# Performance work log

Measured on AMD Instinct MI355X. Metric: run time of the kernel, lower is better.

The kernel has to match this reference:

```python
import jax, jax.numpy as jnp
import numpy as np

NUM_EXPERTS = 8
HIDDEN = 2048
FFN = 1376
CAPACITY_FACTOR = 1.25
SCORE_SCALE = 1.0


def setup_inputs() -> dict:
    key = jax.random.key(0)
    k = jax.random.split(key, 6)
    T = 8192
    x = jax.random.normal(k[0], (T, HIDDEN), dtype=jnp.float32)
    topK_indices = jax.random.randint(k[1], (T,), 0, NUM_EXPERTS, dtype=jnp.int64)
    topK_scores = jax.random.uniform(k[2], (T,), dtype=jnp.float32)
    s = 1.0 / np.sqrt(HIDDEN)
    w_gate = jax.random.normal(k[3], (NUM_EXPERTS, HIDDEN, FFN), dtype=jnp.float32) * s
    w_up = jax.random.normal(k[4], (NUM_EXPERTS, HIDDEN, FFN), dtype=jnp.float32) * s
    w_down = jax.random.normal(k[5], (NUM_EXPERTS, FFN, HIDDEN), dtype=jnp.float32) * (1.0 / np.sqrt(FFN))
    return {"x": x, "topK_indices": topK_indices, "topK_scores": topK_scores,
            "w_gate": w_gate, "w_up": w_up, "w_down": w_down}


def reference(x, topK_indices, topK_scores, w_gate, w_up, w_down):
    T, D = x.shape
    E = w_gate.shape[0]
    capacity = int(CAPACITY_FACTOR * T / E)  # static (depends only on shapes)
    # position of each token within its assigned expert (deterministic drop:
    # keep the first `capacity` tokens in sequence order per expert)
    oh = jax.nn.one_hot(topK_indices, E, dtype=jnp.int32)          # [T,E]
    rank = jnp.take_along_axis(jnp.cumsum(oh, axis=0) - 1,
                               topK_indices[:, None].astype(jnp.int32), axis=1)[:, 0]
    keep = rank < capacity                                          # [T]
    # dispatch into per-expert capacity buffers; dropped tokens go to dummy slot
    slot = jnp.where(keep, topK_indices.astype(jnp.int32) * capacity + rank, E * capacity)
    buf = jnp.zeros((E * capacity + 1, D), x.dtype)
    buf = buf.at[slot].set(jnp.where(keep[:, None], x, jnp.zeros_like(x)))
    xe = buf[:E * capacity].reshape(E, capacity, D)                 # [E,C,D]
    # per-expert SwiGLU MLP as grouped GEMMs
    h = jax.nn.silu(jnp.einsum('ecd,edf->ecf', xe, w_gate)) * jnp.einsum('ecd,edf->ecf', xe, w_up)
    out = jnp.einsum('ecf,efd->ecd', h, w_down).reshape(E * capacity, D)
    out = jnp.concatenate([out, jnp.zeros((1, D), out.dtype)], axis=0)
    # combine: dropped tokens -> zero (dropped_padding='zero'), gate-score fusion
    y = out[slot] * keep[:, None].astype(out.dtype)
    y = y * (topK_scores[:, None] * SCORE_SCALE)
    return y
```

## Files before the change

### kernel.cpp

```cpp
#include <hip/hip_runtime.h>
#include <hip/hip_bf16.h>
#include <cstdint>
#include <cstddef>

#define NTOK 8192
#define DH   2048
#define DF   1376
#define DFP  1408
#define NE   8
#define CAP  1280

typedef __bf16 bf16x8 __attribute__((ext_vector_type(8)));
typedef float  f32x4  __attribute__((ext_vector_type(4)));

#define BARRIER() asm volatile("s_barrier" ::: "memory")
#define WAITV(n)  asm volatile("s_waitcnt vmcnt(" #n ")" ::: "memory")
#define SETPRIO(n) __builtin_amdgcn_s_setprio(n)

__device__ __forceinline__ uint32_t pk2(float a, float b) {
  float2 f; f.x = a; f.y = b;
  union { __hip_bfloat162 h; uint32_t u; } cv;
  cv.h = __float22bfloat162_rn(f);
  return cv.u;
}
__device__ __forceinline__ ushort bf16bits(float a) {
  return (ushort)(pk2(a, 0.f) & 0xFFFFu);
}
__device__ __forceinline__ void gload16(const ushort* g, ushort* l) {
  __builtin_amdgcn_global_load_lds(
      (const __attribute__((address_space(1))) uint32_t*)(const void*)g,
      (__attribute__((address_space(3))) uint32_t*)(void*)l,
      16, 0, 0);
}

__device__ __forceinline__ void rp_src(int o, int& row, int& ko) {
  int p = o >> 7;
  int g = ((o >> 4) & 7) ^ (p & 7);
  row = p * 2 + (g >> 2);
  ko  = (g & 3) * 8;
}
__device__ __forceinline__ int rp_off(int row, int l4) {
  return ((row >> 1) << 7) + (((((row & 1) << 2) + l4) ^ ((row >> 1) & 7)) << 4);
}

__global__ void routing_kernel(const int* __restrict__ idx, int* __restrict__ tok_slot,
                               int* __restrict__ tok_keep) {
  __shared__ int cnt[256][NE];
  const int t = threadIdx.x;
  for (int s = t; s < NE * CAP; s += 256) tok_slot[s] = -1;
  unsigned long long cA = 0ull, cB = 0ull;
  const int per = NTOK / 256, base = t * per;
  for (int i = 0; i < per; ++i) {
    int e = idx[base + i];
    unsigned long long inc = 1ull << ((e & 3) * 16);
    if (e < 4) cA += inc; else cB += inc;
  }
#pragma unroll
  for (int e = 0; e < 4; ++e) cnt[t][e]     = (int)((cA >> (e * 16)) & 0xFFFF);
#pragma unroll
  for (int e = 0; e < 4; ++e) cnt[t][4 + e] = (int)((cB >> (e * 16)) & 0xFFFF);
  __syncthreads();
  if (t < NE) {
    int run = 0;
    for (int i = 0; i < 256; ++i) { int c = cnt[i][t]; cnt[i][t] = run; run += c; }
  }
  __syncthreads();
  cA = 0ull; cB = 0ull;
#pragma unroll
  for (int e = 0; e < 4; ++e) cA |= (unsigned long long)(cnt[t][e] & 0xFFFF) << (e * 16);
#pragma unroll
  for (int e = 0; e < 4; ++e) cB |= (unsigned long long)(cnt[t][4 + e] & 0xFFFF) << (e * 16);
  for (int i = 0; i < per; ++i) {
    int token = base + i;
    int e = idx[token];
    int sh = (e & 3) * 16;
    int r = (int)(((e < 4 ? cA : cB) >> sh) & 0xFFFF);
    unsigned long long inc = 1ull << sh;
    if (e < 4) cA += inc; else cB += inc;
    bool keep = (r < CAP);
    tok_keep[token] = keep ? 1 : 0;
    if (keep) tok_slot[e * CAP + r] = token;
  }
}

__global__ void zero_dropped(const int* __restrict__ keep, float* __restrict__ y) {
  if (keep[blockIdx.x]) return;
  float4 z = {0.f, 0.f, 0.f, 0.f};
  float* p = y + (size_t)blockIdx.x * DH + threadIdx.x * 8;
  *(float4*)p = z;
  *(float4*)(p + 4) = z;
}

__global__ void convert_x(const float* __restrict__ x, ushort* __restrict__ xb) {
  int i = (blockIdx.x * 256 + threadIdx.x) * 8;
  float4 a = *(const float4*)(x + i);
  float4 b = *(const float4*)(x + i + 4);
  uint4 p = { pk2(a.x, a.y), pk2(a.z, a.w), pk2(b.x, b.y), pk2(b.z, b.w) };
  *(uint4*)(xb + i) = p;
}

__global__ __launch_bounds__(256) void transpose_cvt(
    const float* __restrict__ in, ushort* __restrict__ out, int K, int N) {
  __shared__ ushort T[64][72];
  const int tid = threadIdx.x;
  const int n0 = blockIdx.x * 64, k0 = blockIdx.y * 64;
  const size_t eoff_in  = (size_t)blockIdx.z * K * N;
  const size_t eoff_out = (size_t)blockIdx.z * N * K;
  const int kr = tid >> 4;
  const int nc = (tid & 15) * 4;
#pragma unroll
  for (int it = 0; it < 4; ++it) {
    int k = k0 + kr + it * 16;
    int n = n0 + nc;
    float4 v = {0.f, 0.f, 0.f, 0.f};
    if (k < K && n + 4 <= N) v = *(const float4*)(in + eoff_in + (size_t)k * N + n);
    T[nc + 0][kr + it * 16] = bf16bits(v.x);
    T[nc + 1][kr + it * 16] = bf16bits(v.y);
    T[nc + 2][kr + it * 16] = bf16bits(v.z);
    T[nc + 3][kr + it * 16] = bf16bits(v.w);
  }
  __syncthreads();
  const int nr = tid >> 2;
  const int kc = tid & 3;
#pragma unroll
  for (int it = 0; it < 2; ++it) {
    int kloc = kc * 16 + it * 8;
    int n = n0 + nr, k = k0 + kloc;
    if (n < N && k + 8 <= K)
      *(uint4*)(out + eoff_out + (size_t)n * K + k) = *(const uint4*)&T[nr][kloc];
  }
}

__global__ void pad_h(ushort* __restrict__ h) {
  int idx = blockIdx.x * 512 + threadIdx.x;
  int row = idx >> 2, q = idx & 3;
  uint4 z = {0u, 0u, 0u, 0u};
  *(uint4*)(h + (size_t)row * DFP + DF + q * 8) = z;
}

__global__ __launch_bounds__(512, 1) void gemm_gateup3(
    const ushort* __restrict__ xb, const ushort* __restrict__ wgt,
    const ushort* __restrict__ wut, const int* __restrict__ tok_slot,
    ushort* __restrict__ h)
{
  __shared__ __align__(16) char sm[131072];
  const int tid = threadIdx.x, lane = tid & 63, wid = tid >> 6;
  const int wr = wid >> 1, wc = wid & 1;
  const int l15 = lane & 15, l4 = lane >> 4;

  int wgid = (blockIdx.x & 7) * 55 + (blockIdx.x >> 3);
  const int e = wgid / 55;
  const int rem = wgid - e * 55;
  const int mt = rem / 11, nt = rem - (rem / 11) * 11;
  const int n0 = nt * 128;

  const ushort* srcA[2]; const ushort* srcBg; const ushort* srcBu;
#pragma unroll
  for (int c = 0; c < 2; ++c) {
    int o = c * 8192 + wid * 1024 + lane * 16;
    int row, ko; rp_src(o, row, ko);
    int tk = tok_slot[e * CAP + mt * 256 + row];
    if (tk < 0) tk = 0;
    srcA[c] = xb + (size_t)tk * DH + ko;
  }
  {
    int o = wid * 1024 + lane * 16;
    int row, ko; rp_src(o, row, ko);
    int n = n0 + row; if (n > DF - 1) n = DF - 1;
    srcBg = wgt + ((size_t)e * DF + n) * DH + ko;
    srcBu = wut + ((size_t)e * DF + n) * DH + ko;
  }
  int aoff[4], boff[4];
#pragma unroll
  for (int i = 0; i < 4; ++i) aoff[i] = rp_off(wr * 64 + i * 16 + l15, l4);
#pragma unroll
  for (int j = 0; j < 4; ++j) boff[j] = rp_off(wc * 64 + j * 16 + l15, l4);
  const int dstw = wid * 1024;

  f32x4 accG[4][4], accU[4][4];
#pragma unroll
  for (int i = 0; i < 4; ++i)
#pragma unroll
    for (int j = 0; j < 4; ++j) {
      accG[i][j] = (f32x4){0.f, 0.f, 0.f, 0.f};
      accU[i][j] = (f32x4){0.f, 0.f, 0.f, 0.f};
    }

  const int NT = DH / 32;
#pragma unroll
  for (int t0 = 0; t0 < 3; ++t0) {
    int kk = t0 * 32;
    gload16(srcA[0] + kk, (ushort*)(sm + t0 * 16384 + dstw));
    gload16(srcA[1] + kk, (ushort*)(sm + t0 * 16384 + 8192 + dstw));
    gload16(srcBg   + kk, (ushort*)(sm + 65536 + t0 * 8192 + dstw));
    gload16(srcBu   + kk, (ushort*)(sm + 98304 + t0 * 8192 + dstw));
  }
  WAITV(8);
  BARRIER();

  for (int t = 0; t < NT; ++t) {
    const int r = t & 3, w = (t + 3) & 3;
    char* Ab  = sm + r * 16384;
    char* Bgb = sm + 65536 + r * 8192;
    char* Bub = sm + 98304 + r * 8192;
    bf16x8 a[4], bg[4], bu[4];
#pragma unroll
    for (int i = 0; i < 4; ++i) a[i]  = *(const bf16x8*)(Ab + aoff[i]);
#pragma unroll
    for (int j = 0; j < 4; ++j) bg[j] = *(const bf16x8*)(Bgb + boff[j]);
#pragma unroll
    for (int j = 0; j < 4; ++j) bu[j] = *(const bf16x8*)(Bub + boff[j]);
    if (t + 3 < NT) {
      int kk = (t + 3) * 32;
      gload16(srcA[0] + kk, (ushort*)(sm + w * 16384 + dstw));
      gload16(srcA[1] + kk, (ushort*)(sm + w * 16384 + 8192 + dstw));
      gload16(srcBg   + kk, (ushort*)(sm + 65536 + w * 8192 + dstw));
      gload16(srcBu   + kk, (ushort*)(sm + 98304 + w * 8192 + dstw));
    }
    SETPRIO(1);
#pragma unroll
    for (int j = 0; j < 4; ++j)
#pragma unroll
      for (int i = 0; i < 4; ++i)
        accG[i][j] = __builtin_amdgcn_mfma_f32_16x16x32_bf16(a[i], bg[j], accG[i][j], 0, 0, 0);
#pragma unroll
    for (int j = 0; j < 4; ++j)
#pragma unroll
      for (int i = 0; i < 4; ++i)
        accU[i][j] = __builtin_amdgcn_mfma_f32_16x16x32_bf16(a[i], bu[j], accU[i][j], 0, 0, 0);
    SETPRIO(0);
    if (t + 3 < NT)      { WAITV(8); }
    else if (t + 2 < NT) { WAITV(4); }
    else if (t + 1 < NT) { WAITV(0); }
    BARRIER();
  }
  const size_t rowbase = (size_t)(e * CAP + mt * 256 + wr * 64);
#pragma unroll
  for (int j = 0; j < 4; ++j) {
    int col = n0 + wc * 64 + j * 16 + l15;
    if (col < DF) {
#pragma unroll
      for (int i = 0; i < 4; ++i)
#pragma unroll
        for (int r2 = 0; r2 < 4; ++r2) {
          size_t row = rowbase + i * 16 + l4 * 4 + r2;
          float gv = accG[i][j][r2], uv = accU[i][j][r2];
          h[row * DFP + col] = bf16bits(gv / (1.f + __expf(-gv)) * uv);
        }
    }
  }
}

__global__ __launch_bounds__(512, 1) void gemm_down3(
    const ushort* __restrict__ h, const ushort* __restrict__ wdt,
    const int* __restrict__ tok_slot, const float* __restrict__ scores,
    float* __restrict__ y)
{
  __shared__ __align__(16) char sm[100352];
  int* tokc = (int*)(sm + 98304);
  float* scc = (float*)(sm + 99328);
  const int tid = threadIdx.x, lane = tid & 63, wid = tid >> 6;
  const int wr = wid >> 1, wc = wid & 1;
  const int l15 = lane & 15, l4 = lane >> 4;

  int wgid = (blockIdx.x & 7) * 80 + (blockIdx.x >> 3);
  const int e = wgid / 80;
  const int rem = wgid - e * 80;
  const int mt = rem / 16, nt = rem & 15;
  const int n0 = nt * 128;

  if (tid < 256) {
    int tk = tok_slot[e * CAP + mt * 256 + tid];
    tokc[tid] = tk;
    scc[tid] = (tk >= 0) ? scores[tk] : 0.f;
  }
  __syncthreads();

  const size_t hrow0 = (size_t)(e * CAP + mt * 256);
  const ushort* srcA[2]; const ushort* srcB;
#pragma unroll
  for (int c = 0; c < 2; ++c) {
    int o = c * 8192 + wid * 1024 + lane * 16;
    int row, ko; rp_src(o, row, ko);
    srcA[c] = h + (hrow0 + row) * DFP + ko;
  }
  {
    int o = wid * 1024 + lane * 16;
    int row, ko; rp_src(o, row, ko);
    srcB = wdt + ((size_t)e * DH + n0 + row) * DF + ko;
  }
  int aoff[4], boff[4];
#pragma unroll
  for (int i = 0; i < 4; ++i) aoff[i] = rp_off(wr * 64 + i * 16 + l15, l4);
#pragma unroll
  for (int j = 0; j < 4; ++j) boff[j] = rp_off(wc * 64 + j * 16 + l15, l4);
  const int dstw = wid * 1024;

  f32x4 acc[4][4];
#pragma unroll
  for (int i = 0; i < 4; ++i)
#pragma unroll
    for (int j = 0; j < 4; ++j) acc[i][j] = (f32x4){0.f, 0.f, 0.f, 0.f};

  const int NT = DFP / 32;
#pragma unroll
  for (int t0 = 0; t0 < 3; ++t0) {
    int kk = t0 * 32;
    gload16(srcA[0] + kk, (ushort*)(sm + t0 * 16384 + dstw));
    gload16(srcA[1] + kk, (ushort*)(sm + t0 * 16384 + 8192 + dstw));
    gload16(srcB    + kk, (ushort*)(sm + 65536 + t0 * 8192 + dstw));
  }
  WAITV(6);
  BARRIER();

  for (int t = 0; t < NT; ++t) {
    const int r = t & 3, w = (t + 3) & 3;
    char* Ab = sm + r * 16384;
    char* Bb = sm + 65536 + r * 8192;
    bf16x8 a[4], b[4];
#pragma unroll
    for (int i = 0; i < 4; ++i) a[i] = *(const bf16x8*)(Ab + aoff[i]);
#pragma unroll
    for (int j = 0; j < 4; ++j) b[j] = *(const bf16x8*)(Bb + boff[j]);
    if (t + 3 < NT) {
      int kk = (t + 3) * 32;
      gload16(srcA[0] + kk, (ushort*)(sm + w * 16384 + dstw));
      gload16(srcA[1] + kk, (ushort*)(sm + w * 16384 + 8192 + dstw));
      gload16(srcB    + kk, (ushort*)(sm + 65536 + w * 8192 + dstw));
    }
    SETPRIO(1);
#pragma unroll
    for (int j = 0; j < 4; ++j)
#pragma unroll
      for (int i = 0; i < 4; ++i)
        acc[i][j] = __builtin_amdgcn_mfma_f32_16x16x32_bf16(a[i], b[j], acc[i][j], 0, 0, 0);
    SETPRIO(0);
    if (t + 3 < NT)      { WAITV(6); }
    else if (t + 2 < NT) { WAITV(3); }
    else if (t + 1 < NT) { WAITV(0); }
    BARRIER();
  }
  int tkr[4][4]; float sr[4][4];
#pragma unroll
  for (int i = 0; i < 4; ++i)
#pragma unroll
    for (int r = 0; r < 4; ++r) {
      int rl = wr * 64 + i * 16 + l4 * 4 + r;
      tkr[i][r] = tokc[rl];
      sr[i][r]  = scc[rl];
    }
#pragma unroll
  for (int j = 0; j < 4; ++j) {
    int col = n0 + wc * 64 + j * 16 + l15;
#pragma unroll
    for (int i = 0; i < 4; ++i)
#pragma unroll
      for (int r = 0; r < 4; ++r)
        if (tkr[i][r] >= 0)
          y[(size_t)tkr[i][r] * DH + col] = acc[i][j][r] * sr[i][r];
  }
}

extern "C" void kernel_launch(void* const* d_in, const int* in_sizes, int n_in,
                              void* d_out, int out_size, void* d_ws, size_t ws_size,
                              hipStream_t stream) {
  const float* x   = (const float*)d_in[0];
  const int*   idx = (const int*)d_in[1];
  const float* sc  = (const float*)d_in[2];
  const float* wg  = (const float*)d_in[3];
  const float* wu  = (const float*)d_in[4];
  const float* wd  = (const float*)d_in[5];
  float* y = (float*)d_out;

  const size_t OFF_KEEP = 40960;
  const size_t OFF_H    = 73728;
  const size_t SZ_H     = (size_t)NE * CAP * DFP * 2;
  const size_t OFF_XB   = OFF_H + SZ_H;
  const size_t SZ_XB    = (size_t)NTOK * DH * 2;
  const size_t OFF_WGT  = OFF_XB + SZ_XB;
  const size_t SZ_W     = (size_t)NE * DH * DF * 2;
  const size_t OFF_WUT  = OFF_WGT + SZ_W;

  int* tok_slot = (int*)d_ws;
  int* tok_keep = (int*)((char*)d_ws + OFF_KEEP);
  ushort* hbuf = (ushort*)((char*)d_ws + OFF_H);
  ushort* xb   = (ushort*)((char*)d_ws + OFF_XB);
  ushort* wgt  = (ushort*)((char*)d_ws + OFF_WGT);
  ushort* wut  = (ushort*)((char*)d_ws + OFF_WUT);
  ushort* wdt  = wgt;

  hipLaunchKernelGGL(routing_kernel, dim3(1), dim3(256), 0, stream, idx, tok_slot, tok_keep);
  hipLaunchKernelGGL(zero_dropped, dim3(NTOK), dim3(256), 0, stream, tok_keep, y);
  hipLaunchKernelGGL(convert_x, dim3(NTOK * DH / 2048), dim3(256), 0, stream, x, xb);
  hipLaunchKernelGGL(transpose_cvt, dim3((DF + 63) / 64, DH / 64, NE), dim3(256), 0, stream,
                     wg, wgt, DH, DF);
  hipLaunchKernelGGL(transpose_cvt, dim3((DF + 63) / 64, DH / 64, NE), dim3(256), 0, stream,
                     wu, wut, DH, DF);
  hipLaunchKernelGGL(pad_h, dim3(80), dim3(512), 0, stream, hbuf);
  hipLaunchKernelGGL(gemm_gateup3, dim3(440), dim3(512), 0, stream,
                     xb, wgt, wut, tok_slot, hbuf);
  hipLaunchKernelGGL(transpose_cvt, dim3(DH / 64, (DF + 63) / 64, NE), dim3(256), 0, stream,
                     wd, wdt, DF, DH);
  hipLaunchKernelGGL(gemm_down3, dim3(640), dim3(512), 0, stream,
                     hbuf, wdt, tok_slot, sc, y);
}
```

Before: 356.0 us.

## Fuse prep kernels, merge weight transposes, drop h padding, double-buffer GEMM fragments

Merges the x-conversion and dropped-row zeroing into one kernel, and the three weight transposes into a single launch writing to a separate down-weight buffer. Removes the padded h layout and the pad kernel so the down GEMM runs over the exact 1376-wide K (43 tiles). Both GEMM main loops now prefetch the next LDS fragment into a second register set while issuing MFMAs on the current one, with explicit lgkmcnt waits and sched barriers. Launch bounds are raised to 2 waves per SIMD. The aim is fewer launches and less LDS-read latency stall. The cost is higher register pressure from the doubled fragment registers.

Measured after the change: 333.4 us. -6.4%, faster.

```diff
diff --git a/kernel.cpp b/kernel.cpp
--- a/kernel.cpp
+++ b/kernel.cpp
@@ -6,7 +6,6 @@
 #define NTOK 8192
 #define DH   2048
 #define DF   1376
-#define DFP  1408
 #define NE   8
 #define CAP  1280
 
@@ -15,6 +14,8 @@
 
 #define BARRIER() asm volatile("s_barrier" ::: "memory")
 #define WAITV(n)  asm volatile("s_waitcnt vmcnt(" #n ")" ::: "memory")
+#define LGKM(n)   asm volatile("s_waitcnt lgkmcnt(" #n ")" ::: "memory")
+#define SCHED0()  __builtin_amdgcn_sched_barrier(0)
 #define SETPRIO(n) __builtin_amdgcn_s_setprio(n)
 
 __device__ __forceinline__ uint32_t pk2(float a, float b) {
@@ -83,29 +84,36 @@
   }
 }
 
-__global__ void zero_dropped(const int* __restrict__ keep, float* __restrict__ y) {
-  if (keep[blockIdx.x]) return;
-  float4 z = {0.f, 0.f, 0.f, 0.f};
-  float* p = y + (size_t)blockIdx.x * DH + threadIdx.x * 8;
-  *(float4*)p = z;
-  *(float4*)(p + 4) = z;
-}
-
-__global__ void convert_x(const float* __restrict__ x, ushort* __restrict__ xb) {
-  int i = (blockIdx.x * 256 + threadIdx.x) * 8;
-  float4 a = *(const float4*)(x + i);
-  float4 b = *(const float4*)(x + i + 4);
+__global__ void xconv_zero(const float* __restrict__ x, const int* __restrict__ keep,
+                           ushort* __restrict__ xb, float* __restrict__ y) {
+  const int row = blockIdx.x;
+  const int c = threadIdx.x * 8;
+  const size_t off = (size_t)row * DH + c;
+  float4 a = *(const float4*)(x + off);
+  float4 b = *(const float4*)(x + off + 4);
   uint4 p = { pk2(a.x, a.y), pk2(a.z, a.w), pk2(b.x, b.y), pk2(b.z, b.w) };
-  *(uint4*)(xb + i) = p;
-}
-
-__global__ __launch_bounds__(256) void transpose_cvt(
-    const float* __restrict__ in, ushort* __restrict__ out, int K, int N) {
+  *(uint4*)(xb + off) = p;
+  if (!keep[row]) {
+    float4 z = {0.f, 0.f, 0.f, 0.f};
+    *(float4*)(y + off) = z;
+    *(float4*)(y + off + 4) = z;
+  }
+}
+
+__global__ __launch_bounds__(256) void transpose_all(
+    const float* __restrict__ wg, const float* __restrict__ wu, const float* __restrict__ wd,
+    ushort* __restrict__ wgt, ushort* __restrict__ wut, ushort* __restrict__ wdt) {
+  const int z = blockIdx.z;
+  const float* in; ushort* out; int K, N, eidx;
+  if (z < 8)       { in = wg; out = wgt; K = DH; N = DF; eidx = z; }
+  else if (z < 16) { in = wu; out = wut; K = DH; N = DF; eidx = z - 8; }
+  else             { in = wd; out = wdt; K = DF; N = DH; eidx = z - 16; }
+  const int n0 = blockIdx.x * 64, k0 = blockIdx.y * 64;
+  if (n0 >= N || k0 >= K) return;
   __shared__ ushort T[64][72];
   const int tid = threadIdx.x;
-  const int n0 = blockIdx.x * 64, k0 = blockIdx.y * 64;
-  const size_t eoff_in  = (size_t)blockIdx.z * K * N;
-  const size_t eoff_out = (size_t)blockIdx.z * N * K;
+  const size_t eoff_in  = (size_t)eidx * K * N;
+  const size_t eoff_out = (size_t)eidx * N * K;
   const int kr = tid >> 4;
   const int nc = (tid & 15) * 4;
 #pragma unroll
@@ -131,14 +139,40 @@
   }
 }
 
-__global__ void pad_h(ushort* __restrict__ h) {
-  int idx = blockIdx.x * 512 + threadIdx.x;
-  int row = idx >> 2, q = idx & 3;
-  uint4 z = {0u, 0u, 0u, 0u};
-  *(uint4*)(h + (size_t)row * DFP + DF + q * 8) = z;
-}
-
-__global__ __launch_bounds__(512, 1) void gemm_gateup3(
+#define GU_READ(SET, RB) { \
+  char* Ab_  = sm + (RB) * 16384; \
+  char* Bgb_ = sm + 65536 + (RB) * 8192; \
+  char* Bub_ = sm + 98304 + (RB) * 8192; \
+  _Pragma("unroll") for (int i_ = 0; i_ < 4; ++i_) aR##SET[i_]  = *(const bf16x8*)(Ab_ + aoff[i_]); \
+  _Pragma("unroll") for (int j_ = 0; j_ < 4; ++j_) bgR##SET[j_] = *(const bf16x8*)(Bgb_ + boff[j_]); \
+  _Pragma("unroll") for (int j_ = 0; j_ < 4; ++j_) buR##SET[j_] = *(const bf16x8*)(Bub_ + boff[j_]); \
+}
+#define GU_MFMA(SET) { \
+  _Pragma("unroll") for (int j_ = 0; j_ < 4; ++j_) \
+    _Pragma("unroll") for (int i_ = 0; i_ < 4; ++i_) \
+      accG[i_][j_] = __builtin_amdgcn_mfma_f32_16x16x32_bf16(aR##SET[i_], bgR##SET[j_], accG[i_][j_], 0, 0, 0); \
+  _Pragma("unroll") for (int j_ = 0; j_ < 4; ++j_) \
+    _Pragma("unroll") for (int i_ = 0; i_ < 4; ++i_) \
+      accU[i_][j_] = __builtin_amdgcn_mfma_f32_16x16x32_bf16(aR##SET[i_], buR##SET[j_], accU[i_][j_], 0, 0, 0); \
+}
+#define GU_BODY(T, CUR, NXT) { \
+  const int t_ = (T); \
+  if (t_ + 3 < NT) { \
+    const int kk_ = (t_ + 3) * 32; const int w_ = (t_ + 3) & 3; \
+    gload16(srcA[0] + kk_, (ushort*)(sm + w_ * 16384 + dstw)); \
+    gload16(srcA[1] + kk_, (ushort*)(sm + w_ * 16384 + 8192 + dstw)); \
+    gload16(srcBg + kk_, (ushort*)(sm + 65536 + w_ * 8192 + dstw)); \
+    gload16(srcBu + kk_, (ushort*)(sm + 98304 + w_ * 8192 + dstw)); \
+  } \
+  if (t_ + 1 < NT) { GU_READ(NXT, (t_ + 1) & 3); LGKM(12); } else { LGKM(0); } \
+  SCHED0(); SETPRIO(1); \
+  GU_MFMA(CUR); \
+  SETPRIO(0); SCHED0(); \
+  if (t_ + 3 < NT) { WAITV(4); } else if (t_ + 2 < NT) { WAITV(0); } \
+  BARRIER(); \
+}
+
+__global__ __launch_bounds__(512, 2) void gemm_gateup3(
     const ushort* __restrict__ xb, const ushort* __restrict__ wgt,
     const ushort* __restrict__ wut, const int* __restrict__ tok_slot,
     ushort* __restrict__ h)
@@ -195,45 +229,17 @@
     gload16(srcBg   + kk, (ushort*)(sm + 65536 + t0 * 8192 + dstw));
     gload16(srcBu   + kk, (ushort*)(sm + 98304 + t0 * 8192 + dstw));
   }
-  WAITV(8);
+  WAITV(4);
   BARRIER();
 
-  for (int t = 0; t < NT; ++t) {
-    const int r = t & 3, w = (t + 3) & 3;
-    char* Ab  = sm + r * 16384;
-    char* Bgb = sm + 65536 + r * 8192;
-    char* Bub = sm + 98304 + r * 8192;
-    bf16x8 a[4], bg[4], bu[4];
-#pragma unroll
-    for (int i = 0; i < 4; ++i) a[i]  = *(const bf16x8*)(Ab + aoff[i]);
-#pragma unroll
-    for (int j = 0; j < 4; ++j) bg[j] = *(const bf16x8*)(Bgb + boff[j]);
-#pragma unroll
-    for (int j = 0; j < 4; ++j) bu[j] = *(const bf16x8*)(Bub + boff[j]);
-    if (t + 3 < NT) {
-      int kk = (t + 3) * 32;
-      gload16(srcA[0] + kk, (ushort*)(sm + w * 16384 + dstw));
-      gload16(srcA[1] + kk, (ushort*)(sm + w * 16384 + 8192 + dstw));
-      gload16(srcBg   + kk, (ushort*)(sm + 65536 + w * 8192 + dstw));
-      gload16(srcBu   + kk, (ushort*)(sm + 98304 + w * 8192 + dstw));
-    }
-    SETPRIO(1);
-#pragma unroll
-    for (int j = 0; j < 4; ++j)
-#pragma unroll
-      for (int i = 0; i < 4; ++i)
-        accG[i][j] = __builtin_amdgcn_mfma_f32_16x16x32_bf16(a[i], bg[j], accG[i][j], 0, 0, 0);
-#pragma unroll
-    for (int j = 0; j < 4; ++j)
-#pragma unroll
-      for (int i = 0; i < 4; ++i)
-        accU[i][j] = __builtin_amdgcn_mfma_f32_16x16x32_bf16(a[i], bu[j], accU[i][j], 0, 0, 0);
-    SETPRIO(0);
-    if (t + 3 < NT)      { WAITV(8); }
-    else if (t + 2 < NT) { WAITV(4); }
-    else if (t + 1 < NT) { WAITV(0); }
-    BARRIER();
-  }
+  bf16x8 aR0[4], bgR0[4], buR0[4], aR1[4], bgR1[4], buR1[4];
+  GU_READ(0, 0);
+
+  for (int t = 0; t < NT; t += 2) {
+    GU_BODY(t, 0, 1);
+    GU_BODY(t + 1, 1, 0);
+  }
+
   const size_t rowbase = (size_t)(e * CAP + mt * 256 + wr * 64);
 #pragma unroll
   for (int j = 0; j < 4; ++j) {
@@ -245,13 +251,40 @@
         for (int r2 = 0; r2 < 4; ++r2) {
           size_t row = rowbase + i * 16 + l4 * 4 + r2;
           float gv = accG[i][j][r2], uv = accU[i][j][r2];
-          h[row * DFP + col] = bf16bits(gv / (1.f + __expf(-gv)) * uv);
+          h[row * DF + col] = bf16bits(gv / (1.f + __expf(-gv)) * uv);
         }
     }
   }
 }
 
-__global__ __launch_bounds__(512, 1) void gemm_down3(
+#define DN_READ(SET, RB) { \
+  char* Ab_ = sm + (RB) * 16384; \
+  char* Bb_ = sm + 65536 + (RB) * 8192; \
+  _Pragma("unroll") for (int i_ = 0; i_ < 4; ++i_) aR##SET[i_] = *(const bf16x8*)(Ab_ + aoff[i_]); \
+  _Pragma("unroll") for (int j_ = 0; j_ < 4; ++j_) bR##SET[j_] = *(const bf16x8*)(Bb_ + boff[j_]); \
+}
+#define DN_MFMA(SET) { \
+  _Pragma("unroll") for (int j_ = 0; j_ < 4; ++j_) \
+    _Pragma("unroll") for (int i_ = 0; i_ < 4; ++i_) \
+      acc[i_][j_] = __builtin_amdgcn_mfma_f32_16x16x32_bf16(aR##SET[i_], bR##SET[j_], acc[i_][j_], 0, 0, 0); \
+}
+#define DN_BODY(T, CUR, NXT) { \
+  const int t_ = (T); \
+  if (t_ + 3 < NT) { \
+    const int kk_ = (t_ + 3) * 32; const int w_ = (t_ + 3) & 3; \
+    gload16(srcA[0] + kk_, (ushort*)(sm + w_ * 16384 + dstw)); \
+    gload16(srcA[1] + kk_, (ushort*)(sm + w_ * 16384 + 8192 + dstw)); \
+    gload16(srcB + kk_, (ushort*)(sm + 65536 + w_ * 8192 + dstw)); \
+  } \
+  if (t_ + 1 < NT) { DN_READ(NXT, (t_ + 1) & 3); LGKM(8); } else { LGKM(0); } \
+  SCHED0(); SETPRIO(1); \
+  DN_MFMA(CUR); \
+  SETPRIO(0); SCHED0(); \
+  if (t_ + 3 < NT) { WAITV(3); } else if (t_ + 2 < NT) { WAITV(0); } \
+  BARRIER(); \
+}
+
+__global__ __launch_bounds__(512, 2) void gemm_down3(
     const ushort* __restrict__ h, const ushort* __restrict__ wdt,
     const int* __restrict__ tok_slot, const float* __restrict__ scores,
     float* __restrict__ y)
@@ -282,7 +315,7 @@
   for (int c = 0; c < 2; ++c) {
     int o = c * 8192 + wid * 1024 + lane * 16;
     int row, ko; rp_src(o, row, ko);
-    srcA[c] = h + (hrow0 + row) * DFP + ko;
+    srcA[c] = h + (hrow0 + row) * DF + ko;
   }
   {
     int o = wid * 1024 + lane * 16;
@@ -302,7 +335,7 @@
 #pragma unroll
     for (int j = 0; j < 4; ++j) acc[i][j] = (f32x4){0.f, 0.f, 0.f, 0.f};
 
-  const int NT = DFP / 32;
+  const int NT = DF / 32;
 #pragma unroll
   for (int t0 = 0; t0 < 3; ++t0) {
     int kk = t0 * 32;
@@ -310,36 +343,18 @@
     gload16(srcA[1] + kk, (ushort*)(sm + t0 * 16384 + 8192 + dstw));
     gload16(srcB    + kk, (ushort*)(sm + 65536 + t0 * 8192 + dstw));
   }
-  WAITV(6);
+  WAITV(3);
   BARRIER();
 
-  for (int t = 0; t < NT; ++t) {
-    const int r = t & 3, w = (t + 3) & 3;
-    char* Ab = sm + r * 16384;
-    char* Bb = sm + 65536 + r * 8192;
-    bf16x8 a[4], b[4];
-#pragma unroll
-    for (int i = 0; i < 4; ++i) a[i] = *(const bf16x8*)(Ab + aoff[i]);
-#pragma unroll
-    for (int j = 0; j < 4; ++j) b[j] = *(const bf16x8*)(Bb + boff[j]);
-    if (t + 3 < NT) {
-      int kk = (t + 3) * 32;
-      gload16(srcA[0] + kk, (ushort*)(sm + w * 16384 + dstw));
-      gload16(srcA[1] + kk, (ushort*)(sm + w * 16384 + 8192 + dstw));
-      gload16(srcB    + kk, (ushort*)(sm + 65536 + w * 8192 + dstw));
-    }
-    SETPRIO(1);
-#pragma unroll
-    for (int j = 0; j < 4; ++j)
-#pragma unroll
-      for (int i = 0; i < 4; ++i)
-        acc[i][j] = __builtin_amdgcn_mfma_f32_16x16x32_bf16(a[i], b[j], acc[i][j], 0, 0, 0);
-    SETPRIO(0);
-    if (t + 3 < NT)      { WAITV(6); }
-    else if (t + 2 < NT) { WAITV(3); }
-    else if (t + 1 < NT) { WAITV(0); }
-    BARRIER();
-  }
+  bf16x8 aR0[4], bR0[4], aR1[4], bR1[4];
+  DN_READ(0, 0);
+
+  for (int t = 0; t < NT - 1; t += 2) {
+    DN_BODY(t, 0, 1);
+    DN_BODY(t + 1, 1, 0);
+  }
+  DN_BODY(NT - 1, 0, 1);
+
   int tkr[4][4]; float sr[4][4];
 #pragma unroll
   for (int i = 0; i < 4; ++i)
@@ -374,12 +389,13 @@
 
   const size_t OFF_KEEP = 40960;
   const size_t OFF_H    = 73728;
-  const size_t SZ_H     = (size_t)NE * CAP * DFP * 2;
+  const size_t SZ_H     = (size_t)NE * CAP * DF * 2;
   const size_t OFF_XB   = OFF_H + SZ_H;
   const size_t SZ_XB    = (size_t)NTOK * DH * 2;
   const size_t OFF_WGT  = OFF_XB + SZ_XB;
   const size_t SZ_W     = (size_t)NE * DH * DF * 2;
   const size_t OFF_WUT  = OFF_WGT + SZ_W;
+  const size_t OFF_WDT  = OFF_WUT + SZ_W;
 
   int* tok_slot = (int*)d_ws;
   int* tok_keep = (int*)((char*)d_ws + OFF_KEEP);
@@ -387,20 +403,14 @@
   ushort* xb   = (ushort*)((char*)d_ws + OFF_XB);
   ushort* wgt  = (ushort*)((char*)d_ws + OFF_WGT);
   ushort* wut  = (ushort*)((char*)d_ws + OFF_WUT);
-  ushort* wdt  = wgt;
+  ushort* wdt  = (ushort*)((char*)d_ws + OFF_WDT);
 
   hipLaunchKernelGGL(routing_kernel, dim3(1), dim3(256), 0, stream, idx, tok_slot, tok_keep);
-  hipLaunchKernelGGL(zero_dropped, dim3(NTOK), dim3(256), 0, stream, tok_keep, y);
-  hipLaunchKernelGGL(convert_x, dim3(NTOK * DH / 2048), dim3(256), 0, stream, x, xb);
-  hipLaunchKernelGGL(transpose_cvt, dim3((DF + 63) / 64, DH / 64, NE), dim3(256), 0, stream,
-                     wg, wgt, DH, DF);
-  hipLaunchKernelGGL(transpose_cvt, dim3((DF + 63) / 64, DH / 64, NE), dim3(256), 0, stream,
-                     wu, wut, DH, DF);
-  hipLaunchKernelGGL(pad_h, dim3(80), dim3(512), 0, stream, hbuf);
+  hipLaunchKernelGGL(xconv_zero, dim3(NTOK), dim3(256), 0, stream, x, tok_keep, xb, y);
+  hipLaunchKernelGGL(transpose_all, dim3(32, 32, 24), dim3(256), 0, stream,
+                     wg, wu, wd, wgt, wut, wdt);
   hipLaunchKernelGGL(gemm_gateup3, dim3(440), dim3(512), 0, stream,
                      xb, wgt, wut, tok_slot, hbuf);
-  hipLaunchKernelGGL(transpose_cvt, dim3(DH / 64, (DF + 63) / 64, NE), dim3(256), 0, stream,
-                     wd, wdt, DF, DH);
   hipLaunchKernelGGL(gemm_down3, dim3(640), dim3(512), 0, stream,
                      hbuf, wdt, tok_slot, sc, y);
 }
```
